# Kernel optimization log

Hardware: AMD Instinct MI355X
Metric: run time of the kernel (lower is better)

## Reference

```python
import jax, jax.numpy as jnp
import numpy as np
from jax import lax

B, C_IN, C_OUT, H, W = 32, 96, 96, 56, 56
E = 8          # num_experts
HID = 576      # round(96 * 6)
K = 3          # depthwise kernel size


def setup_inputs() -> dict:
    key = jax.random.key(0)
    ks = jax.random.split(key, 12)
    f = lambda k, s, sc=0.05: jax.random.normal(k, s, dtype=jnp.float32) * sc
    return {
        "x": jax.random.normal(ks[0], (B, C_IN, H, W), dtype=jnp.float32),
        # router for expand conv (input = x, C_IN channels)
        "w_r1": f(ks[1], (E, C_IN)), "b_r1": jnp.zeros((E,), jnp.float32),
        # expert bank for 1x1 expand: [E, HID, C_IN]
        "w1": f(ks[2], (E, HID, C_IN)),
        "g1": jnp.ones((HID,), jnp.float32), "bt1": jnp.zeros((HID,), jnp.float32),
        "m1": f(ks[3], (HID,), 0.01), "v1": jax.random.uniform(ks[4], (HID,), dtype=jnp.float32) + 0.5,
        # router for depthwise conv (input = expanded features, HID channels)
        "w_r2": f(ks[5], (E, HID)), "b_r2": jnp.zeros((E,), jnp.float32),
        # expert bank for depthwise 3x3: [E, HID, K, K] (in/groups = 1)
        "w2": f(ks[6], (E, HID, K, K)),
        "g2": jnp.ones((HID,), jnp.float32), "bt2": jnp.zeros((HID,), jnp.float32),
        "m2": f(ks[7], (HID,), 0.01), "v2": jax.random.uniform(ks[8], (HID,), dtype=jnp.float32) + 0.5,
        # expert bank for 1x1 project: [E, C_OUT, HID]
        "w3": f(ks[9], (E, C_OUT, HID)),
        "g3": jnp.ones((C_OUT,), jnp.float32), "bt3": jnp.zeros((C_OUT,), jnp.float32),
        "m3": f(ks[10], (C_OUT,), 0.01), "v3": jax.random.uniform(ks[11], (C_OUT,), dtype=jnp.float32) + 0.5,
        # block-level router (input = x, C_IN channels) gating the project conv
        "w_r3": f(jax.random.fold_in(key, 99), (E, C_IN)), "b_r3": jnp.zeros((E,), jnp.float32),
    }


def _route(feat, Wf, bf):
    # BasicRouter: global avg pool -> Linear -> sigmoid. feat: [B, C, H, W] -> [B, E]
    return jax.nn.sigmoid(feat.mean(axis=(2, 3)) @ Wf.T + bf)


def _bn(y, g, b, m, v, eps=1e-5):
    inv = g * lax.rsqrt(v + eps)
    return y * inv[None, :, None, None] + (b - m * inv)[None, :, None, None]


def reference(x, w_r1, b_r1, w1, g1, bt1, m1, v1,
              w_r2, b_r2, w2, g2, bt2, m2, v2,
              w3, g3, bt3, m3, v3, w_r3, b_r3):
    r1 = _route(x, w_r1, b_r1)      # [B, E] gate for expand conv
    r_blk = _route(x, w_r3, b_r3)   # [B, E] block router gates project conv

    # --- CondConv 1x1 expand: per-sample mixed kernel as batched GEMM ---
    w1c = jnp.einsum('be,eoc->boc', r1, w1)              # [B, HID, C_IN]
    y = jnp.einsum('bchw,boc->bohw', x, w1c)             # [B, HID, H, W]
    y = jnp.clip(_bn(y, g1, bt1, m1, v1), 0.0, 6.0)      # ReLU6

    # --- CondConv depthwise 3x3 (groups = HID), router on expanded feats ---
    r2 = _route(y, w_r2, b_r2)                           # [B, E]
    kw = jnp.einsum('be,eckl->bckl', r2, w2).reshape(B * HID, 1, K, K)
    y = lax.conv_general_dilated(
        y.reshape(1, B * HID, H, W), kw, (1, 1), 'SAME',
        dimension_numbers=('NCHW', 'OIHW', 'NCHW'),
        feature_group_count=B * HID).reshape(B, HID, H, W)
    y = jnp.clip(_bn(y, g2, bt2, m2, v2), 0.0, 6.0)

    # --- CondConv 1x1 project, gated by the block router(x) ---
    w3c = jnp.einsum('be,eoc->boc', r_blk, w3)           # [B, C_OUT, HID]
    y = jnp.einsum('bchw,boc->bohw', y, w3c)             # [B, C_OUT, H, W]
    y = _bn(y, g3, bt3, m3, v3)

    return x + y  # stride==1 and inp==oup -> residual connection
```

## Files before the change

kernel.cpp:

```cpp
#include <hip/hip_runtime.h>
#include <hip/hip_bf16.h>

#define B_   32
#define CIN  96
#define COUT 96
#define NP   3136
#define NE   8
#define HIDD 576

typedef short bf16x8 __attribute__((ext_vector_type(8)));
typedef float f32x4 __attribute__((ext_vector_type(4)));

__device__ __forceinline__ unsigned short f2bf(float f) {
  __hip_bfloat16 h = __float2bfloat16(f);
  unsigned short u; __builtin_memcpy(&u, &h, 2); return u;
}
__device__ __forceinline__ float u2f(unsigned int v) {
  float f; __builtin_memcpy(&f, &v, 4); return f;
}

__global__ __launch_bounds__(256) void k_transpose(const float* __restrict__ x,
                                                   unsigned short* __restrict__ xt,
                                                   float* __restrict__ xpart) {
  __shared__ float tile[CIN][65];
  int bi = blockIdx.x; int b = bi / 49, pt = bi % 49; int p0 = pt * 64;
  int t = threadIdx.x;
  for (int j = t; j < CIN * 64; j += 256) {
    int c = j >> 6, pi = j & 63;
    tile[c][pi] = x[((size_t)(b * CIN + c)) * NP + p0 + pi];
  }
  __syncthreads();
  if (t < CIN) {
    float s = 0.f;
    for (int i = 0; i < 64; ++i) s += tile[t][i];
    xpart[((size_t)(b * 49 + pt)) * CIN + t] = s;
  }
  for (int j = t; j < 64 * CIN; j += 256) {
    int p = j / CIN, c = j % CIN;
    xt[((size_t)(b * NP + p0 + p)) * CIN + c] = f2bf(tile[c][p]);
  }
}

__global__ __launch_bounds__(64) void k_front(const float* __restrict__ xpart,
    const float* __restrict__ wr1, const float* __restrict__ br1,
    const float* __restrict__ wr3, const float* __restrict__ br3,
    float* __restrict__ r1, float* __restrict__ rblk,
    const float* g1, const float* bt1, const float* m1, const float* v1,
    const float* g2, const float* bt2, const float* m2, const float* v2,
    const float* g3, const float* bt3, const float* m3, const float* v3,
    float* sc1, float* bi1, float* sc2, float* bi2, float* sc3, float* bi3) {
  int bi = blockIdx.x; int lane = threadIdx.x;
  if (bi < 512) {
    const float* wr; const float* br; float* dst; int id;
    if (bi < 256) { wr = wr1; br = br1; dst = r1;   id = bi; }
    else          { wr = wr3; br = br3; dst = rblk; id = bi - 256; }
    int b = id >> 3, e = id & 7;
    float s = 0.f;
    for (int c = lane; c < CIN; c += 64) {
      const float* xp = xpart + (size_t)b * 49 * CIN + c;
      float xm = 0.f;
#pragma unroll 7
      for (int k = 0; k < 49; ++k) xm += xp[k * CIN];
      s += xm * (1.0f / NP) * wr[e * CIN + c];
    }
    s += __shfl_xor(s, 1);  s += __shfl_xor(s, 2);  s += __shfl_xor(s, 4);
    s += __shfl_xor(s, 8);  s += __shfl_xor(s, 16); s += __shfl_xor(s, 32);
    if (lane == 0) dst[id] = 1.0f / (1.0f + __expf(-(s + br[e])));
  } else {
    int i = (bi - 512) * 64 + lane;
    if (i < HIDD) {
      float s = g1[i] * rsqrtf(v1[i] + 1e-5f); sc1[i] = s; bi1[i] = bt1[i] - m1[i] * s;
    } else if (i < 2 * HIDD) {
      int c = i - HIDD;
      float s = g2[c] * rsqrtf(v2[c] + 1e-5f); sc2[c] = s; bi2[c] = bt2[c] - m2[c] * s;
    } else if (i < 2 * HIDD + COUT) {
      int c = i - 2 * HIDD;
      float s = g3[c] * rsqrtf(v3[c] + 1e-5f); sc3[c] = s; bi3[c] = bt3[c] - m3[c] * s;
    }
  }
}

__global__ __launch_bounds__(256) void k_mixw(
    const float* __restrict__ w1, const float* __restrict__ r1, unsigned short* __restrict__ w1c,
    const float* __restrict__ w3, const float* __restrict__ rblk, unsigned short* __restrict__ w3c) {
  __shared__ float rsh[256];
  int bi = blockIdx.x; int t = threadIdx.x;
  const float* w; const float* r; unsigned short* dst; int oc0;
  if (bi < 216) { w = w1; r = r1;   dst = w1c; oc0 = bi * 256; }
  else          { w = w3; r = rblk; dst = w3c; oc0 = (bi - 216) * 256; }
  rsh[t] = r[t];
  __syncthreads();
  int oc = oc0 + t;
  float wv[NE];
#pragma unroll
  for (int e = 0; e < NE; ++e) wv[e] = w[(size_t)e * 55296 + oc];
  for (int b = 0; b < B_; ++b) {
    float a = 0.f;
#pragma unroll
    for (int e = 0; e < NE; ++e) a += rsh[b * 8 + e] * wv[e];
    dst[(size_t)b * 55296 + oc] = f2bf(a);
  }
}

__global__ __launch_bounds__(256) void k_expand2(const unsigned short* __restrict__ xt,
    const unsigned short* __restrict__ w1c, const float* __restrict__ sc1,
    const float* __restrict__ bi1, unsigned short* __restrict__ y2,
    float* __restrict__ yspart) {
  __shared__ unsigned short As[64 * 104];
  __shared__ unsigned short Bs[64 * 104];
  int t = threadIdx.x;
  int pt = blockIdx.x;
  int p0 = pt * 64, o0 = blockIdx.y * 64, b = blockIdx.z;
  const unsigned short* ag = w1c + (size_t)b * 55296 + (size_t)o0 * 96;
  const unsigned short* bg = xt + ((size_t)b * NP + p0) * 96;
  for (int j = t; j < 768; j += 256) {
    int r = j / 12, ch = j % 12;
    *(int4*)(As + r * 104 + ch * 8) = *(const int4*)(ag + r * 96 + ch * 8);
    *(int4*)(Bs + r * 104 + ch * 8) = *(const int4*)(bg + r * 96 + ch * 8);
  }
  __syncthreads();
  int lane = t & 63, wv = t >> 6;
  int m = lane & 15, q = lane >> 4;
  f32x4 acc[4];
#pragma unroll
  for (int nt = 0; nt < 4; ++nt) acc[nt] = 0.f;
#pragma unroll
  for (int kk = 0; kk < 3; ++kk) {
    bf16x8 af = *(const bf16x8*)(As + (wv * 16 + m) * 104 + kk * 32 + q * 8);
#pragma unroll
    for (int nt = 0; nt < 4; ++nt) {
      bf16x8 bfb = *(const bf16x8*)(Bs + (nt * 16 + m) * 104 + kk * 32 + q * 8);
      acc[nt] = __builtin_amdgcn_mfma_f32_16x16x32_bf16(af, bfb, acc[nt], 0, 0, 0);
    }
  }
  __syncthreads();
  float sc[4], bb[4];
#pragma unroll
  for (int i = 0; i < 4; ++i) {
    int o = o0 + wv * 16 + q * 4 + i;
    sc[i] = sc1[o]; bb[i] = bi1[o];
  }
  float rs[4] = {0.f, 0.f, 0.f, 0.f};
  unsigned short* T = As;
#pragma unroll
  for (int nt = 0; nt < 4; ++nt) {
    unsigned short pk[4];
#pragma unroll
    for (int i = 0; i < 4; ++i) {
      float v = acc[nt][i] * sc[i] + bb[i];
      v = fminf(fmaxf(v, 0.f), 6.f);
      rs[i] += v;
      pk[i] = f2bf(v);
    }
    uint2 pv; __builtin_memcpy(&pv, pk, 8);
    *(uint2*)(T + (nt * 16 + m) * 72 + wv * 16 + q * 4) = pv;
  }
#pragma unroll
  for (int i = 0; i < 4; ++i) {
    float r = rs[i];
    r += __shfl_xor(r, 1); r += __shfl_xor(r, 2);
    r += __shfl_xor(r, 4); r += __shfl_xor(r, 8);
    if (m == 0)
      yspart[((size_t)b * 49 + pt) * HIDD + o0 + wv * 16 + q * 4 + i] = r;
  }
  __syncthreads();
  for (int j = t; j < 512; j += 256) {
    int r = j >> 3, ch = j & 7;
    *(int4*)(y2 + ((size_t)(b * NP + p0 + r)) * 576 + o0 + ch * 8) =
        *(const int4*)(T + r * 72 + ch * 8);
  }
}

__global__ __launch_bounds__(256) void k_mid(const float* __restrict__ yspart,
    const float* __restrict__ wr2, const float* __restrict__ br2,
    const float* __restrict__ w2, const float* __restrict__ sc2,
    const float* __restrict__ bi2, float* __restrict__ kwt) {
  __shared__ float ysum_l[HIDD];
  __shared__ float r2_l[NE];
  int b = blockIdx.x, t = threadIdx.x;
  const float* yp = yspart + (size_t)b * 49 * HIDD;
  for (int c = t; c < HIDD; c += 256) {
    float s = 0.f;
#pragma unroll 7
    for (int k = 0; k < 49; ++k) s += yp[k * HIDD + c];
    ysum_l[c] = s;
  }
  __syncthreads();
  int wv = t >> 6, lane = t & 63;
  for (int e = wv; e < NE; e += 4) {
    float s = 0.f;
    for (int h = lane; h < HIDD; h += 64)
      s += ysum_l[h] * (1.0f / NP) * wr2[e * HIDD + h];
    s += __shfl_xor(s, 1);  s += __shfl_xor(s, 2);  s += __shfl_xor(s, 4);
    s += __shfl_xor(s, 8);  s += __shfl_xor(s, 16); s += __shfl_xor(s, 32);
    if (lane == 0) r2_l[e] = 1.0f / (1.0f + __expf(-(s + br2[e])));
  }
  __syncthreads();
  float rr[NE];
#pragma unroll
  for (int e = 0; e < NE; ++e) rr[e] = r2_l[e];
  for (int c = t; c < HIDD; c += 256) {
    float sc = sc2[c];
    float* dst = kwt + (size_t)b * 5760 + c;
#pragma unroll
    for (int k = 0; k < 9; ++k) {
      float s = 0.f;
#pragma unroll
      for (int e = 0; e < NE; ++e) s += rr[e] * w2[((size_t)e * HIDD + c) * 9 + k];
      dst[k * 576] = s * sc;
    }
    dst[9 * 576] = bi2[c];
  }
}

__device__ __forceinline__ f32x4 cvt4(uint2 v) {
  f32x4 r;
  r[0] = u2f(v.x << 16); r[1] = u2f(v.x & 0xffff0000u);
  r[2] = u2f(v.y << 16); r[3] = u2f(v.y & 0xffff0000u);
  return r;
}
__device__ __forceinline__ uint2 pack4(f32x4 v) {
  uint2 r;
  r.x = (unsigned)f2bf(v[0]) | ((unsigned)f2bf(v[1]) << 16);
  r.y = (unsigned)f2bf(v[2]) | ((unsigned)f2bf(v[3]) << 16);
  return r;
}
__device__ __forceinline__ f32x4 clamp6(f32x4 v) {
#pragma unroll
  for (int i = 0; i < 4; ++i) v[i] = fminf(fmaxf(v[i], 0.f), 6.f);
  return v;
}

__global__ __launch_bounds__(512, 4) void k_dwproj(const unsigned short* __restrict__ y2,
    const float* __restrict__ kwt, const unsigned short* __restrict__ w3c,
    const float* __restrict__ sc3, const float* __restrict__ bi3,
    const float* __restrict__ x, float* __restrict__ out) {
  __shared__ unsigned short zl[56 * 584];
  __shared__ unsigned short As[96 * 72];
  int t = threadIdx.x;
  int hr = blockIdx.x, b = blockIdx.z;
  int h = (hr & 7) * 7 + (hr >> 3);
  const unsigned short* ag = w3c + (size_t)b * 55296;

  int r0 = t >> 3, c8 = t & 7;
  int r1 = 64 + (t >> 3);
  bool two = (t < 256);
  int4 ra0, ra1;
#define LOADA(kc) do {                                                       \
    ra0 = *(const int4*)(ag + (size_t)r0 * 576 + (kc) * 64 + c8 * 8);        \
    if (two) ra1 = *(const int4*)(ag + (size_t)r1 * 576 + (kc) * 64 + c8 * 8); \
  } while (0)
#define WRITEA() do {                                                        \
    *(int4*)(As + r0 * 72 + c8 * 8) = ra0;                                   \
    if (two) *(int4*)(As + r1 * 72 + c8 * 8) = ra1;                          \
  } while (0)

  LOADA(0);

  {
    bool okU = (h > 0), okD = (h < 55);
    int rU = okU ? (h - 1) : h;
    int rD = okD ? (h + 1) : h;
    f32x4 d0, d1, d2;
#pragma unroll 1
    for (int task = t; task < 576; task += 512) {
      int cgi = task % 144;
      int seg = task / 144;
      int c = cgi * 4, w0 = seg * 14;
      const float* kp = kwt + (size_t)b * 5760 + c;
      f32x4 tk[9], tb;
#pragma unroll
      for (int k = 0; k < 9; ++k) tk[k] = *(const f32x4*)(kp + k * 576);
      tb = *(const f32x4*)(kp + 9 * 576);
      const unsigned short* yrU = y2 + ((size_t)(b * NP + rU * 56)) * 576 + c;
      const unsigned short* yrC = y2 + ((size_t)(b * NP + h  * 56)) * 576 + c;
      const unsigned short* yrD = y2 + ((size_t)(b * NP + rD * 56)) * 576 + c;

#define LOADC3(j) do {                                                       \
      uint2 q0, q1, q2;                                                      \
      q0.x = q0.y = q1.x = q1.y = q2.x = q2.y = 0u;                          \
      if ((unsigned)(j) < 56u) {                                             \
        if (okU) q0 = *(const uint2*)(yrU + (size_t)(j) * 576);              \
        q1 = *(const uint2*)(yrC + (size_t)(j) * 576);                       \
        if (okD) q2 = *(const uint2*)(yrD + (size_t)(j) * 576);              \
      }                                                                      \
      d0 = cvt4(q0); d1 = cvt4(q1); d2 = cvt4(q2);                           \
    } while (0)

#define SCAT3(A, Bv, Cv, j, STORE) do {                                      \
      LOADC3(j);                                                             \
      A  += d0 * tk[2] + d1 * tk[5] + d2 * tk[8];                            \
      Bv += d0 * tk[1] + d1 * tk[4] + d2 * tk[7];                            \
      Cv += d0 * tk[0] + d1 * tk[3] + d2 * tk[6];                            \
      if (STORE)                                                             \
        *(uint2*)(zl + (size_t)((j) - 1) * 584 + c) = pack4(clamp6(A));      \
      A = tb;                                                                \
    } while (0)

      f32x4 Av = tb, Bv = tb, Cv = tb;
      SCAT3(Av, Bv, Cv, w0 - 1, false);
      SCAT3(Bv, Cv, Av, w0,     false);
#pragma unroll 1
      for (int u = 0; u < 4; ++u) {
        int j = w0 + 1 + u * 3;
        SCAT3(Cv, Av, Bv, j,     true);
        SCAT3(Av, Bv, Cv, j + 1, true);
        SCAT3(Bv, Cv, Av, j + 2, true);
      }
      SCAT3(Cv, Av, Bv, w0 + 13, true);
      LOADC3(w0 + 14);
      Av += d0 * tk[2] + d1 * tk[5] + d2 * tk[8];
      *(uint2*)(zl + (size_t)(w0 + 13) * 584 + c) = pack4(clamp6(Av));
#undef SCAT3
#undef LOADC3
    }
  }

  WRITEA();
  __syncthreads();

  int lane = t & 63, wv = t >> 6;
  int wr = wv >> 2, wc = wv & 3;
  int m = lane & 15, q = lane >> 4;
  int px = wc * 16 + m;
  int pxr = (px < 56) ? px : 55;
  f32x4 acc0, acc1, acc2;
  acc0 = 0.f; acc1 = 0.f; acc2 = 0.f;

#define COMPUTE(kc) do {                                                     \
    _Pragma("unroll") for (int kk = 0; kk < 2; ++kk) {                       \
      bf16x8 bfv = *(const bf16x8*)(zl + (size_t)pxr * 584 + (kc) * 64 + kk * 32 + q * 8); \
      bf16x8 af0 = *(const bf16x8*)(As + (wr * 48 +  0 + m) * 72 + kk * 32 + q * 8); \
      bf16x8 af1 = *(const bf16x8*)(As + (wr * 48 + 16 + m) * 72 + kk * 32 + q * 8); \
      bf16x8 af2 = *(const bf16x8*)(As + (wr * 48 + 32 + m) * 72 + kk * 32 + q * 8); \
      acc0 = __builtin_amdgcn_mfma_f32_16x16x32_bf16(af0, bfv, acc0, 0, 0, 0); \
      acc1 = __builtin_amdgcn_mfma_f32_16x16x32_bf16(af1, bfv, acc1, 0, 0, 0); \
      acc2 = __builtin_amdgcn_mfma_f32_16x16x32_bf16(af2, bfv, acc2, 0, 0, 0); \
    } } while (0)

#pragma unroll 1
  for (int kc = 0; kc < 8; ++kc) {
    LOADA(kc + 1);
    COMPUTE(kc);
    __syncthreads();
    WRITEA();
    __syncthreads();
  }
  COMPUTE(8);

#undef COMPUTE
#undef LOADA
#undef WRITEA

  if (px < 56) {
    size_t pbase = (size_t)b * COUT * NP + (size_t)h * 56 + px;
#define EPI(ACC, a) do {                                                     \
    _Pragma("unroll") for (int i = 0; i < 4; ++i) {                          \
      int o = wr * 48 + (a) * 16 + q * 4 + i;                                \
      size_t idx = pbase + (size_t)o * NP;                                   \
      out[idx] = ACC[i] * sc3[o] + bi3[o] + x[idx];                          \
    } } while (0)
    EPI(acc0, 0); EPI(acc1, 1); EPI(acc2, 2);
#undef EPI
  }
}

#define OFF_XT     ((size_t)0)
#define OFF_KWT    OFF_XT
#define OFF_Y      ((size_t)19267584)
#define OFF_Z      ((size_t)134873088)
#define OFF_XPART  OFF_Z
#define OFF_YSPART (OFF_Z + 602112)
#define OFF_W1C    ((size_t)250478592)
#define OFF_W3C    ((size_t)254017536)
#define OFF_R1     ((size_t)257642496)
#define OFF_RBLK   ((size_t)257643520)
#define OFF_SC1    ((size_t)257645568)
#define OFF_BI1    ((size_t)257647872)
#define OFF_SC2    ((size_t)257650176)
#define OFF_BI2    ((size_t)257652480)
#define OFF_SC3    ((size_t)257654784)
#define OFF_BI3    ((size_t)257655168)

extern "C" void kernel_launch(void* const* d_in, const int* in_sizes, int n_in,
                              void* d_out, int out_size, void* d_ws, size_t ws_size,
                              hipStream_t stream) {
  const float* x   = (const float*)d_in[0];
  const float* wr1 = (const float*)d_in[1];
  const float* br1 = (const float*)d_in[2];
  const float* w1  = (const float*)d_in[3];
  const float* g1  = (const float*)d_in[4];
  const float* bt1 = (const float*)d_in[5];
  const float* m1  = (const float*)d_in[6];
  const float* v1  = (const float*)d_in[7];
  const float* wr2 = (const float*)d_in[8];
  const float* br2 = (const float*)d_in[9];
  const float* w2  = (const float*)d_in[10];
  const float* g2  = (const float*)d_in[11];
  const float* bt2 = (const float*)d_in[12];
  const float* m2  = (const float*)d_in[13];
  const float* v2  = (const float*)d_in[14];
  const float* w3  = (const float*)d_in[15];
  const float* g3  = (const float*)d_in[16];
  const float* bt3 = (const float*)d_in[17];
  const float* m3  = (const float*)d_in[18];
  const float* v3  = (const float*)d_in[19];
  const float* wr3 = (const float*)d_in[20];
  const float* br3 = (const float*)d_in[21];
  float* out = (float*)d_out;
  char* ws = (char*)d_ws;

  unsigned short* xt     = (unsigned short*)(ws + OFF_XT);
  unsigned short* y2     = (unsigned short*)(ws + OFF_Y);
  unsigned short* w1c    = (unsigned short*)(ws + OFF_W1C);
  unsigned short* w3c    = (unsigned short*)(ws + OFF_W3C);
  float* xpart  = (float*)(ws + OFF_XPART);
  float* yspart = (float*)(ws + OFF_YSPART);
  float* r1     = (float*)(ws + OFF_R1);
  float* rblk   = (float*)(ws + OFF_RBLK);
  float* sc1    = (float*)(ws + OFF_SC1);
  float* bi1    = (float*)(ws + OFF_BI1);
  float* sc2    = (float*)(ws + OFF_SC2);
  float* bi2    = (float*)(ws + OFF_BI2);
  float* sc3    = (float*)(ws + OFF_SC3);
  float* bi3    = (float*)(ws + OFF_BI3);
  float* kwt    = (float*)(ws + OFF_KWT);

  k_transpose<<<32 * 49, 256, 0, stream>>>(x, xt, xpart);
  k_front<<<532, 64, 0, stream>>>(xpart, wr1, br1, wr3, br3, r1, rblk,
                                  g1, bt1, m1, v1, g2, bt2, m2, v2, g3, bt3, m3, v3,
                                  sc1, bi1, sc2, bi2, sc3, bi3);
  k_mixw<<<432, 256, 0, stream>>>(w1, r1, w1c, w3, rblk, w3c);
  k_expand2<<<dim3(49, 9, 32), 256, 0, stream>>>(xt, w1c, sc1, bi1, y2, yspart);
  k_mid<<<32, 256, 0, stream>>>(yspart, wr2, br2, w2, sc2, bi2, kwt);
  k_dwproj<<<dim3(56, 1, 32), 512, 0, stream>>>(y2, kwt, w3c, sc3, bi3, x, out);
}
```

Before: 288.3 us.

## Interleave depthwise conv chunks with projection GEMM using double-buffered LDS

Replaces the up-front depthwise pass over all 576 channels (stored in a large LDS tile) with per-64-channel chunks. Each chunk is computed while the projection MFMA for the previous chunk runs, with both the depthwise output and the weight tile double-buffered. This cuts LDS use from about 79KB to about 44KB, which allows a higher occupancy hint, and removes one barrier per iteration. In exchange the depthwise loads become scalar 2-byte bf16 loads per thread instead of 4-channel vector loads, and the kernel weights are reloaded for each chunk.

```diff
diff --git a/kernel.cpp b/kernel.cpp
--- a/kernel.cpp
+++ b/kernel.cpp
@@ -14,6 +14,10 @@
 __device__ __forceinline__ unsigned short f2bf(float f) {
   __hip_bfloat16 h = __float2bfloat16(f);
   unsigned short u; __builtin_memcpy(&u, &h, 2); return u;
+}
+__device__ __forceinline__ float bf2f(unsigned short u) {
+  unsigned int v = ((unsigned int)u) << 16;
+  float f; __builtin_memcpy(&f, &v, 4); return f;
 }
 __device__ __forceinline__ float u2f(unsigned int v) {
   float f; __builtin_memcpy(&f, &v, 4); return f;
@@ -213,30 +217,12 @@
   }
 }
 
-__device__ __forceinline__ f32x4 cvt4(uint2 v) {
-  f32x4 r;
-  r[0] = u2f(v.x << 16); r[1] = u2f(v.x & 0xffff0000u);
-  r[2] = u2f(v.y << 16); r[3] = u2f(v.y & 0xffff0000u);
-  return r;
-}
-__device__ __forceinline__ uint2 pack4(f32x4 v) {
-  uint2 r;
-  r.x = (unsigned)f2bf(v[0]) | ((unsigned)f2bf(v[1]) << 16);
-  r.y = (unsigned)f2bf(v[2]) | ((unsigned)f2bf(v[3]) << 16);
-  return r;
-}
-__device__ __forceinline__ f32x4 clamp6(f32x4 v) {
-#pragma unroll
-  for (int i = 0; i < 4; ++i) v[i] = fminf(fmaxf(v[i], 0.f), 6.f);
-  return v;
-}
-
-__global__ __launch_bounds__(512, 4) void k_dwproj(const unsigned short* __restrict__ y2,
+__global__ __launch_bounds__(512, 6) void k_dwproj2(const unsigned short* __restrict__ y2,
     const float* __restrict__ kwt, const unsigned short* __restrict__ w3c,
     const float* __restrict__ sc3, const float* __restrict__ bi3,
     const float* __restrict__ x, float* __restrict__ out) {
-  __shared__ unsigned short zl[56 * 584];
-  __shared__ unsigned short As[96 * 72];
+  __shared__ unsigned short zbuf[2 * 56 * 72];
+  __shared__ unsigned short As[2 * 96 * 72];
   int t = threadIdx.x;
   int hr = blockIdx.x, b = blockIdx.z;
   int h = (hr & 7) * 7 + (hr >> 3);
@@ -246,78 +232,59 @@
   int r1 = 64 + (t >> 3);
   bool two = (t < 256);
   int4 ra0, ra1;
-#define LOADA(kc) do {                                                       \
-    ra0 = *(const int4*)(ag + (size_t)r0 * 576 + (kc) * 64 + c8 * 8);        \
+#define LOADA(kc) do {                                                        \
+    ra0 = *(const int4*)(ag + (size_t)r0 * 576 + (kc) * 64 + c8 * 8);         \
     if (two) ra1 = *(const int4*)(ag + (size_t)r1 * 576 + (kc) * 64 + c8 * 8); \
   } while (0)
-#define WRITEA() do {                                                        \
-    *(int4*)(As + r0 * 72 + c8 * 8) = ra0;                                   \
-    if (two) *(int4*)(As + r1 * 72 + c8 * 8) = ra1;                          \
+#define WRITEA(kc) do {                                                       \
+    unsigned short* ad = As + ((kc) & 1) * (96 * 72);                         \
+    *(int4*)(ad + r0 * 72 + c8 * 8) = ra0;                                    \
+    if (two) *(int4*)(ad + r1 * 72 + c8 * 8) = ra1;                           \
   } while (0)
 
-  LOADA(0);
-
-  {
-    bool okU = (h > 0), okD = (h < 55);
-    int rU = okU ? (h - 1) : h;
-    int rD = okD ? (h + 1) : h;
-    f32x4 d0, d1, d2;
-#pragma unroll 1
-    for (int task = t; task < 576; task += 512) {
-      int cgi = task % 144;
-      int seg = task / 144;
-      int c = cgi * 4, w0 = seg * 14;
-      const float* kp = kwt + (size_t)b * 5760 + c;
-      f32x4 tk[9], tb;
-#pragma unroll
-      for (int k = 0; k < 9; ++k) tk[k] = *(const f32x4*)(kp + k * 576);
-      tb = *(const f32x4*)(kp + 9 * 576);
-      const unsigned short* yrU = y2 + ((size_t)(b * NP + rU * 56)) * 576 + c;
-      const unsigned short* yrC = y2 + ((size_t)(b * NP + h  * 56)) * 576 + c;
-      const unsigned short* yrD = y2 + ((size_t)(b * NP + rD * 56)) * 576 + c;
-
-#define LOADC3(j) do {                                                       \
-      uint2 q0, q1, q2;                                                      \
-      q0.x = q0.y = q1.x = q1.y = q2.x = q2.y = 0u;                          \
-      if ((unsigned)(j) < 56u) {                                             \
-        if (okU) q0 = *(const uint2*)(yrU + (size_t)(j) * 576);              \
-        q1 = *(const uint2*)(yrC + (size_t)(j) * 576);                       \
-        if (okD) q2 = *(const uint2*)(yrD + (size_t)(j) * 576);              \
-      }                                                                      \
-      d0 = cvt4(q0); d1 = cvt4(q1); d2 = cvt4(q2);                           \
-    } while (0)
-
-#define SCAT3(A, Bv, Cv, j, STORE) do {                                      \
-      LOADC3(j);                                                             \
-      A  += d0 * tk[2] + d1 * tk[5] + d2 * tk[8];                            \
-      Bv += d0 * tk[1] + d1 * tk[4] + d2 * tk[7];                            \
-      Cv += d0 * tk[0] + d1 * tk[3] + d2 * tk[6];                            \
-      if (STORE)                                                             \
-        *(uint2*)(zl + (size_t)((j) - 1) * 584 + c) = pack4(clamp6(A));      \
-      A = tb;                                                                \
-    } while (0)
-
-      f32x4 Av = tb, Bv = tb, Cv = tb;
-      SCAT3(Av, Bv, Cv, w0 - 1, false);
-      SCAT3(Bv, Cv, Av, w0,     false);
-#pragma unroll 1
-      for (int u = 0; u < 4; ++u) {
-        int j = w0 + 1 + u * 3;
-        SCAT3(Cv, Av, Bv, j,     true);
-        SCAT3(Av, Bv, Cv, j + 1, true);
-        SCAT3(Bv, Cv, Av, j + 2, true);
-      }
-      SCAT3(Cv, Av, Bv, w0 + 13, true);
-      LOADC3(w0 + 14);
-      Av += d0 * tk[2] + d1 * tk[5] + d2 * tk[8];
-      *(uint2*)(zl + (size_t)(w0 + 13) * 584 + c) = pack4(clamp6(Av));
-#undef SCAT3
-#undef LOADC3
-    }
-  }
-
-  WRITEA();
-  __syncthreads();
+  int chl = t & 63, seg = t >> 6;
+  bool okU = (h > 0), okD = (h < 55);
+  int rU = okU ? (h - 1) : h;
+  int rD = okD ? (h + 1) : h;
+
+#define DWCHUNK(ck) do {                                                      \
+    int ch = (ck) * 64 + chl;                                                 \
+    const float* kp = kwt + (size_t)b * 5760 + ch;                            \
+    float tk0 = kp[0], tk1 = kp[576], tk2 = kp[1152];                         \
+    float tk3 = kp[1728], tk4 = kp[2304], tk5 = kp[2880];                     \
+    float tk6 = kp[3456], tk7 = kp[4032], tk8 = kp[4608];                     \
+    float tbv = kp[5184];                                                     \
+    const unsigned short* yU = y2 + ((size_t)(b * NP + rU * 56)) * 576 + ch;  \
+    const unsigned short* yC = y2 + ((size_t)(b * NP + h  * 56)) * 576 + ch;  \
+    const unsigned short* yD = y2 + ((size_t)(b * NP + rD * 56)) * 576 + ch;  \
+    unsigned short* zb = zbuf + ((ck) & 1) * (56 * 72) + chl;                 \
+    float o0 = tbv, o1 = tbv, o2 = tbv;                                       \
+    float dU, dC, dD;                                                         \
+    _Pragma("unroll")                                                         \
+    for (int j = 0; j < 9; ++j) {                                             \
+      int w = seg * 7 - 1 + j;                                                \
+      dU = 0.f; dC = 0.f; dD = 0.f;                                           \
+      if ((unsigned)w < 56u) {                                                \
+        if (okU) dU = bf2f(yU[(size_t)w * 576]);                              \
+        dC = bf2f(yC[(size_t)w * 576]);                                       \
+        if (okD) dD = bf2f(yD[(size_t)w * 576]);                              \
+      }                                                                       \
+      float* A; float* Bp; float* Cp;                                         \
+      switch (j % 3) {                                                        \
+        case 0: A = &o0; Bp = &o1; Cp = &o2; break;                           \
+        case 1: A = &o1; Bp = &o2; Cp = &o0; break;                           \
+        default: A = &o2; Bp = &o0; Cp = &o1; break;                          \
+      }                                                                       \
+      *A  += dU * tk2 + dC * tk5 + dD * tk8;                                  \
+      *Bp += dU * tk1 + dC * tk4 + dD * tk7;                                  \
+      *Cp += dU * tk0 + dC * tk3 + dD * tk6;                                  \
+      if (j >= 2) {                                                           \
+        float v = fminf(fmaxf(*A, 0.f), 6.f);                                 \
+        zb[(size_t)(w - 1) * 72] = f2bf(v);                                   \
+      }                                                                       \
+      *A = tbv;      \
+    }                                                                         \
+  } while (0)
 
   int lane = t & 63, wv = t >> 6;
   int wr = wv >> 2, wc = wv & 3;
@@ -327,38 +294,46 @@
   f32x4 acc0, acc1, acc2;
   acc0 = 0.f; acc1 = 0.f; acc2 = 0.f;
 
-#define COMPUTE(kc) do {                                                     \
-    _Pragma("unroll") for (int kk = 0; kk < 2; ++kk) {                       \
-      bf16x8 bfv = *(const bf16x8*)(zl + (size_t)pxr * 584 + (kc) * 64 + kk * 32 + q * 8); \
-      bf16x8 af0 = *(const bf16x8*)(As + (wr * 48 +  0 + m) * 72 + kk * 32 + q * 8); \
-      bf16x8 af1 = *(const bf16x8*)(As + (wr * 48 + 16 + m) * 72 + kk * 32 + q * 8); \
-      bf16x8 af2 = *(const bf16x8*)(As + (wr * 48 + 32 + m) * 72 + kk * 32 + q * 8); \
+#define COMPUTE(kc) do {                                                      \
+    const unsigned short* ab = As + ((kc) & 1) * (96 * 72);                   \
+    const unsigned short* zr = zbuf + ((kc) & 1) * (56 * 72);                 \
+    _Pragma("unroll") for (int kk = 0; kk < 2; ++kk) {                        \
+      bf16x8 bfv = *(const bf16x8*)(zr + pxr * 72 + kk * 32 + q * 8);         \
+      bf16x8 af0 = *(const bf16x8*)(ab + (wr * 48 +  0 + m) * 72 + kk * 32 + q * 8); \
+      bf16x8 af1 = *(const bf16x8*)(ab + (wr * 48 + 16 + m) * 72 + kk * 32 + q * 8); \
+      bf16x8 af2 = *(const bf16x8*)(ab + (wr * 48 + 32 + m) * 72 + kk * 32 + q * 8); \
       acc0 = __builtin_amdgcn_mfma_f32_16x16x32_bf16(af0, bfv, acc0, 0, 0, 0); \
       acc1 = __builtin_amdgcn_mfma_f32_16x16x32_bf16(af1, bfv, acc1, 0, 0, 0); \
       acc2 = __builtin_amdgcn_mfma_f32_16x16x32_bf16(af2, bfv, acc2, 0, 0, 0); \
     } } while (0)
 
+  LOADA(0);
+  DWCHUNK(0);
+  WRITEA(0);
+  __syncthreads();
+
 #pragma unroll 1
   for (int kc = 0; kc < 8; ++kc) {
     LOADA(kc + 1);
+    DWCHUNK(kc + 1);
     COMPUTE(kc);
+    WRITEA(kc + 1);
     __syncthreads();
-    WRITEA();
-    __syncthreads();
   }
   COMPUTE(8);
 
 #undef COMPUTE
+#undef DWCHUNK
 #undef LOADA
 #undef WRITEA
 
   if (px < 56) {
     size_t pbase = (size_t)b * COUT * NP + (size_t)h * 56 + px;
-#define EPI(ACC, a) do {                                                     \
-    _Pragma("unroll") for (int i = 0; i < 4; ++i) {                          \
-      int o = wr * 48 + (a) * 16 + q * 4 + i;                                \
-      size_t idx = pbase + (size_t)o * NP;                                   \
-      out[idx] = ACC[i] * sc3[o] + bi3[o] + x[idx];                          \
+#define EPI(ACC, a) do {                                                      \
+    _Pragma("unroll") for (int i = 0; i < 4; ++i) {                           \
+      int o = wr * 48 + (a) * 16 + q * 4 + i;                                 \
+      size_t idx = pbase + (size_t)o * NP;                                    \
+      out[idx] = ACC[i] * sc3[o] + bi3[o] + x[idx];                           \
     } } while (0)
     EPI(acc0, 0); EPI(acc1, 1); EPI(acc2, 2);
 #undef EPI
@@ -433,5 +408,5 @@
   k_mixw<<<432, 256, 0, stream>>>(w1, r1, w1c, w3, rblk, w3c);
   k_expand2<<<dim3(49, 9, 32), 256, 0, stream>>>(xt, w1c, sc1, bi1, y2, yspart);
   k_mid<<<32, 256, 0, stream>>>(yspart, wr2, br2, w2, sc2, bi2, kwt);
-  k_dwproj<<<dim3(56, 1, 32), 512, 0, stream>>>(y2, kwt, w3c, sc3, bi3, x, out);
-}
+  k_dwproj2<<<dim3(56, 1, 32), 512, 0, stream>>>(y2, kwt, w3c, sc3, bi3, x, out);
+}
```

Result: slower. 553.3 us (+92.0%).
